# Optimization experiments

Measured on AMD Instinct MI355X. Metric: run time of the kernel, lower is better.

## Reference

```python
import jax, jax.numpy as jnp
import numpy as np

EMBED = 1024
HEADS = 16
HEAD_DIM = EMBED // HEADS


def setup_inputs() -> dict:
    key = jax.random.key(0)
    ks = jax.random.split(key, 9)
    N, L = 2, 2048
    inp = {
        "values": jax.random.normal(ks[0], (N, L, EMBED), dtype=jnp.float32),
        "keys": jax.random.normal(ks[1], (N, L, EMBED), dtype=jnp.float32),
        "query": jax.random.normal(ks[2], (N, L, EMBED), dtype=jnp.float32),
        "mask": jax.random.randint(ks[3], (N, 1, L, L), 0, 2, dtype=jnp.int32),
        # per-head projection weights (torch Linear: y = x @ W.T), bias=False
        "Wv": jax.random.normal(ks[4], (HEAD_DIM, HEAD_DIM), dtype=jnp.float32) / np.sqrt(HEAD_DIM),
        "Wk": jax.random.normal(ks[5], (HEAD_DIM, HEAD_DIM), dtype=jnp.float32) / np.sqrt(HEAD_DIM),
        "Wq": jax.random.normal(ks[6], (HEAD_DIM, HEAD_DIM), dtype=jnp.float32) / np.sqrt(HEAD_DIM),
        "Wo": jax.random.normal(ks[7], (EMBED, EMBED), dtype=jnp.float32) / np.sqrt(EMBED),
        "bo": jax.random.normal(ks[8], (EMBED,), dtype=jnp.float32) * 0.02,
    }
    return inp


def reference(values, keys, query, mask, Wv, Wk, Wq, Wo, bo):
    N, Lq = query.shape[0], query.shape[1]
    Lk = keys.shape[1]
    # reshape to (N, L, H, D)
    v = values.reshape(N, Lk, HEADS, HEAD_DIM)
    k = keys.reshape(N, Lk, HEADS, HEAD_DIM)
    q = query.reshape(N, Lq, HEADS, HEAD_DIM)
    # per-head_dim linear projections (shared across heads): x @ W.T
    v = jnp.einsum('nlhd,ed->nlhe', v, Wv)
    k = jnp.einsum('nlhd,ed->nlhe', k, Wk)
    q = jnp.einsum('nqhd,ed->nqhe', q, Wq)
    # scores [N, H, Lq, Lk]
    energy = jnp.einsum('nqhd,nkhd->nhqk', q, k) / np.sqrt(HEAD_DIM).astype(np.float32)
    energy = jnp.where(mask == 0, jnp.float32(-1e20), energy)
    attn = jax.nn.softmax(energy, axis=-1)
    out = jnp.einsum('nhql,nlhd->nqhd', attn, v).reshape(N, Lq, EMBED)
    return out @ Wo.T + bo
```

## Files before the change

### kernel.cpp

```cpp
#include <hip/hip_runtime.h>
#include <hip/hip_bf16.h>

#define SEQ 2048
#define NH 16
#define DH 64
#define EMB 1024

typedef __bf16 bf16;
typedef __attribute__((ext_vector_type(8))) __bf16 bf16x8;
typedef __attribute__((ext_vector_type(4))) __bf16 bf16x4;
typedef __attribute__((ext_vector_type(4))) float f32x4;
typedef __attribute__((ext_vector_type(4))) unsigned int u32x4;
typedef unsigned long long u64;

#define OFF_MQK  0
#define OFF_WO2  8192
#define OFF_K2   (8192 + 2097152)
#define OFF_VT   (OFF_K2 + 8388608)
#define OFF_A2   (OFF_VT + 8388608)
#define OFF_MB   (OFF_A2 + 8388608)

#define LOG2E 1.44269504088896340736f

__device__ __forceinline__ f32x4 mfma16(bf16x8 a, bf16x8 b, f32x4 c) {
  return __builtin_amdgcn_mfma_f32_16x16x32_bf16(a, b, c, 0, 0, 0);
}

#define GL16(g, l)                                                            \
  __builtin_amdgcn_global_load_lds(                                           \
      (const __attribute__((address_space(1))) void*)(g),                     \
      (__attribute__((address_space(3))) void*)(l), 16, 0, 0)

__device__ __forceinline__ unsigned pack_bf16(float p0, float p1) {
  unsigned short b0 = __builtin_bit_cast(unsigned short, (bf16)p0);
  unsigned short b1 = __builtin_bit_cast(unsigned short, (bf16)p1);
  return (unsigned)b0 | ((unsigned)b1 << 16);
}

__global__ __launch_bounds__(256) void prep0(const float* __restrict__ Wq,
                                             const float* __restrict__ Wk,
                                             bf16* __restrict__ mqk) {
  __shared__ float wq[64 * 64];
  __shared__ float wk[64 * 64];
  int tid = threadIdx.x;
  for (int i = tid; i < 4096; i += 256) { wq[i] = Wq[i]; wk[i] = Wk[i]; }
  __syncthreads();
  for (int idx = tid; idx < 4096; idx += 256) {
    int d1 = idx >> 6, d2 = idx & 63;
    float s = 0.f;
#pragma unroll
    for (int e = 0; e < 64; ++e) s += wq[e * 64 + d1] * wk[e * 64 + d2];
    mqk[idx] = (bf16)(s * 0.125f * LOG2E);
  }
}

__global__ __launch_bounds__(256) void prep_fused(
    const float* __restrict__ Wo, const float* __restrict__ Wv,
    const float* __restrict__ keys, const bf16* __restrict__ mqk,
    const float* __restrict__ values, const int* __restrict__ mask,
    bf16* __restrict__ wo2f, bf16* __restrict__ k2f, bf16* __restrict__ vtf,
    u64* __restrict__ mbt) {
  __shared__ __align__(16) float smem[5184];
  int blk = blockIdx.x;
  int tid = threadIdx.x;

  if (blk < 1024) {
    int e = blk;
    float* wv = smem;
    float* worow = smem + 4096;
    for (int i = tid; i < 4096; i += 256) wv[i] = Wv[i];
    for (int i = tid; i < 1024; i += 256) worow[i] = Wo[(size_t)e * 1024 + i];
    __syncthreads();
    int c0 = tid * 4;
    bf16x4 w;
#pragma unroll
    for (int j = 0; j < 4; ++j) {
      int col = c0 + j;
      int hb = col & ~63, dp = col & 63;
      float s = 0.f;
#pragma unroll
      for (int d = 0; d < 64; ++d) s += worow[hb + d] * wv[d * 64 + dp];
      w[j] = (bf16)s;
    }
    int et = e >> 6, t = (e >> 4) & 3, cc = e & 15;
    int kc = c0 >> 5, gg = (c0 >> 3) & 3, half = (c0 >> 2) & 1;
    char* dst = (char*)wo2f + ((size_t)(et * 32 + kc)) * 4096 + t * 1024 +
                (gg * 16 + cc) * 16 + 8 * half;
    *(bf16x4*)dst = w;
  } else if (blk < 2048) {
    int b = blk - 1024;
    int lt = b & 31, h = (b >> 5) & 15, n = b >> 9;
    int wave = tid >> 6, lane = tid & 63;
    int g = lane >> 4, c = lane & 15;
    bf16x8 am[4][2];
#pragma unroll
    for (int t = 0; t < 4; ++t)
#pragma unroll
      for (int s = 0; s < 2; ++s)
        am[t][s] = *(const bf16x8*)(mqk + (16 * t + c) * 64 + 32 * s + 8 * g);
    int l = lt * 64 + wave * 16 + c;
    const float* krow = keys + ((size_t)(n * SEQ + l)) * EMB + h * DH;
    bf16x8 bfr[2];
#pragma unroll
    for (int s = 0; s < 2; ++s) {
      f32x4 x0 = *(const f32x4*)(krow + 32 * s + 8 * g);
      f32x4 x1 = *(const f32x4*)(krow + 32 * s + 8 * g + 4);
      bf16x8 t;
#pragma unroll
      for (int i = 0; i < 4; ++i) { t[i] = (bf16)x0[i]; t[4 + i] = (bf16)x1[i]; }
      bfr[s] = t;
    }
    char* tb = (char*)k2f + (size_t)((n * NH + h) * 32 + lt) * 8192 + wave * 2048;
#pragma unroll
    for (int t = 0; t < 4; ++t) {
      f32x4 a = {0.f, 0.f, 0.f, 0.f};
      a = mfma16(am[t][0], bfr[0], a);
      a = mfma16(am[t][1], bfr[1], a);
      bf16x4 w;
#pragma unroll
      for (int r = 0; r < 4; ++r) w[r] = (bf16)a[r];
      char* dst = tb + (t >> 1) * 1024 +
                  ((2 * (t & 1) + (g >> 1)) * 16 + c) * 16 + 8 * (g & 1);
      *(bf16x4*)dst = w;
    }
  } else if (blk < 3072) {
    int b = blk - 2048;
    int lt = b & 31, h = (b >> 5) & 15, n = b >> 9;
    float (*lds)[65] = (float(*)[65])smem;
    {
      int r = tid >> 2, cg = (tid & 3) * 16;
      const float* vrow =
          values + ((size_t)(n * SEQ + lt * 64 + r)) * EMB + h * DH + cg;
#pragma unroll
      for (int j = 0; j < 16; j += 4) {
        f32x4 x = *(const f32x4*)(vrow + j);
        lds[r][cg + j + 0] = x[0];
        lds[r][cg + j + 1] = x[1];
        lds[r][cg + j + 2] = x[2];
        lds[r][cg + j + 3] = x[3];
      }
    }
    __syncthreads();
    {
      int d = tid >> 2, q16 = tid & 3, lb = q16 * 16;
      bf16x8 w0, w1;
#pragma unroll
      for (int j = 0; j < 8; ++j) w0[j] = (bf16)lds[lb + j][d];
#pragma unroll
      for (int j = 0; j < 8; ++j) w1[j] = (bf16)lds[lb + 8 + j][d];
      int dt = d >> 4, cc = d & 15;
      int s = q16 >> 1, gg = 2 * (q16 & 1);
      char* base = (char*)vtf + (size_t)((n * NH + h) * 32 + lt) * 8192 +
                   (2 * dt + s) * 1024;
      *(bf16x8*)(base + (gg * 16 + cc) * 16) = w0;
      *(bf16x8*)(base + ((gg + 1) * 16 + cc) * 16) = w1;
    }
  } else {
    int base = (blk - 3072) * 4 + (tid >> 6);
    int lane = tid & 63;
#pragma unroll
    for (int i = 0; i < 16; ++i) {
      int w = base + i * 8192;
      int v = mask[(size_t)w * 64 + lane];
      u64 bbits = __ballot(v != 0);
      int kw = w & 31, q = (w >> 5) & 2047, nn = w >> 16;
      if (lane == 0) mbt[((size_t)nn * 32 + kw) * 2048 + q] = bbits;
    }
  }
}

__global__ __launch_bounds__(64, 2) void attn(const float* __restrict__ qraw,
                                              const bf16* __restrict__ k2f,
                                              const bf16* __restrict__ vtf,
                                              const u64* __restrict__ mbt,
                                              bf16* __restrict__ a2) {
  int swz = ((blockIdx.x & 7) << 8) | (blockIdx.x >> 3);
  int qt = swz & 63, h = (swz >> 6) & 15, n = swz >> 10;
  int lane = threadIdx.x, g = lane >> 4, c = lane & 15;

  __shared__ u64 lutm[16];
  if (lane < 16) {
    unsigned a = (lane & 1 ? 0xFFFFu : 0u) | (lane & 2 ? 0xFFFF0000u : 0u);
    unsigned b = (lane & 4 ? 0xFFFFu : 0u) | (lane & 8 ? 0xFFFF0000u : 0u);
    lutm[lane] = (u64)a | ((u64)b << 32);
  }
  __syncthreads();

  bf16x8 qf[2][2];
#pragma unroll
  for (int qi = 0; qi < 2; ++qi) {
    int q = qt * 32 + qi * 16 + c;
    const float* qrow = qraw + ((size_t)(n * SEQ + q)) * EMB + h * DH;
#pragma unroll
    for (int s = 0; s < 2; ++s) {
      f32x4 x0 = *(const f32x4*)(qrow + 32 * s + 8 * g);
      f32x4 x1 = *(const f32x4*)(qrow + 32 * s + 8 * g + 4);
      bf16x8 t;
#pragma unroll
      for (int i = 0; i < 4; ++i) { t[i] = (bf16)x0[i]; t[4 + i] = (bf16)x1[i]; }
      qf[qi][s] = t;
    }
  }
  const char* kp = (const char*)k2f + (size_t)(n * NH + h) * 32 * 8192 + lane * 16;
  const char* vp = (const char*)vtf + (size_t)(n * NH + h) * 32 * 8192 + lane * 16;
  const u64* mq = mbt + (size_t)n * 32 * 2048 + qt * 32 + c;

  bf16x8 K[8], Vv[8];
#pragma unroll
  for (int j = 0; j < 8; ++j) K[j] = *(const bf16x8*)(kp + j * 1024);

  f32x4 oacc[2][4];
#pragma unroll
  for (int qi = 0; qi < 2; ++qi)
#pragma unroll
    for (int dt = 0; dt < 4; ++dt) oacc[qi][dt] = (f32x4){0.f, 0.f, 0.f, 0.f};
  float mrun[2] = {-1e30f, -1e30f}, lrun[2] = {0.f, 0.f};
  bf16x8 ones;
#pragma unroll
  for (int i = 0; i < 8; ++i) ones[i] = (bf16)1.0f;
  int sh0 = 4 * g, sh1 = sh0 + 16;
  int srcA = ((g & 1) << 5) | c;
  int srcB = srcA + 16;
  bool hi2 = (g >> 1) != 0;

  for (int kt = 0; kt < 32; ++kt) {
#pragma unroll
    for (int j = 0; j < 8; ++j)
      Vv[j] = *(const bf16x8*)(vp + (size_t)kt * 8192 + j * 1024);
    u64 mw0 = mq[kt * 2048];
    u64 mw1 = mq[kt * 2048 + 16];

    f32x4 sacc[2][4];
#pragma unroll
    for (int t = 0; t < 4; ++t) {
      bf16x8 k0 = K[2 * t], k1 = K[2 * t + 1];
#pragma unroll
      for (int qi = 0; qi < 2; ++qi) {
        f32x4 a = {0.f, 0.f, 0.f, 0.f};
        a = mfma16(k0, qf[qi][0], a);
        a = mfma16(k1, qf[qi][1], a);
        sacc[qi][t] = a;
      }
    }
#pragma unroll
    for (int j = 0; j < 8; ++j)
      K[j] = *(const bf16x8*)(kp + (size_t)(kt + 1) * 8192 + j * 1024);

    float tmax[2];
#pragma unroll
    for (int qi = 0; qi < 2; ++qi) {
      float x0 = sacc[qi][0][0], x1 = sacc[qi][0][1], x2 = sacc[qi][0][2],
            x3 = sacc[qi][0][3], x4 = sacc[qi][1][0], x5 = sacc[qi][1][1],
            x6 = sacc[qi][1][2], x7 = sacc[qi][1][3], x8 = sacc[qi][2][0],
            x9 = sacc[qi][2][1], xa = sacc[qi][2][2], xb = sacc[qi][2][3],
            xc = sacc[qi][3][0], xd = sacc[qi][3][1], xe = sacc[qi][3][2],
            xf = sacc[qi][3][3];
      float t0 = fmaxf(fmaxf(x0, x1), x2);
      float t1 = fmaxf(fmaxf(x3, x4), x5);
      float t2 = fmaxf(fmaxf(x6, x7), x8);
      float t3 = fmaxf(fmaxf(x9, xa), xb);
      float t4 = fmaxf(fmaxf(xc, xd), xe);
      float m = fmaxf(fmaxf(fmaxf(t0, t1), t2), fmaxf(fmaxf(t3, t4), xf));
      m = fmaxf(m, __shfl_xor(m, 16));
      m = fmaxf(m, __shfl_xor(m, 32));
      tmax[qi] = m;
    }
    bool needs = (tmax[0] > mrun[0] + 8.f) || (tmax[1] > mrun[1] + 8.f);
    if (__any(needs)) {
#pragma unroll
      for (int qi = 0; qi < 2; ++qi) {
        float mnew = fmaxf(mrun[qi], tmax[qi]);
        float scl = __builtin_amdgcn_exp2f(mrun[qi] - mnew);
        lrun[qi] *= scl;
#pragma unroll
        for (int dt = 0; dt < 4; ++dt) {
          oacc[qi][dt][0] *= scl; oacc[qi][dt][1] *= scl;
          oacc[qi][dt][2] *= scl; oacc[qi][dt][3] *= scl;
        }
        mrun[qi] = mnew;
      }
    }
    unsigned wpk[2][4][2];
    u64 mwa[2] = {mw0, mw1};
#pragma unroll
    for (int qi = 0; qi < 2; ++qi) {
      unsigned mlo = (unsigned)mwa[qi], mhi = (unsigned)(mwa[qi] >> 32);
      u64 L[4];
      L[0] = lutm[(mlo >> sh0) & 15];
      L[1] = lutm[(mlo >> sh1) & 15];
      L[2] = lutm[(mhi >> sh0) & 15];
      L[3] = lutm[(mhi >> sh1) & 15];
      float mr = mrun[qi];
#pragma unroll
      for (int t = 0; t < 4; ++t) {
        float p0 = __builtin_amdgcn_exp2f(sacc[qi][t][0] - mr);
        float p1 = __builtin_amdgcn_exp2f(sacc[qi][t][1] - mr);
        float p2 = __builtin_amdgcn_exp2f(sacc[qi][t][2] - mr);
        float p3 = __builtin_amdgcn_exp2f(sacc[qi][t][3] - mr);
        wpk[qi][t][0] = pack_bf16(p0, p1) & (unsigned)L[t];
        wpk[qi][t][1] = pack_bf16(p2, p3) & (unsigned)(L[t] >> 32);
      }
    }
    bf16x8 pf[2][2];
#pragma unroll
    for (int qi = 0; qi < 2; ++qi)
#pragma unroll
      for (int s = 0; s < 2; ++s) {
        unsigned ta0 = (unsigned)__shfl((int)wpk[qi][2 * s][0], srcA);
        unsigned ta1 = (unsigned)__shfl((int)wpk[qi][2 * s][1], srcA);
        unsigned tb0 = (unsigned)__shfl((int)wpk[qi][2 * s + 1][0], srcA);
        unsigned tb1 = (unsigned)__shfl((int)wpk[qi][2 * s + 1][1], srcA);
        unsigned ua0 = (unsigned)__shfl((int)wpk[qi][2 * s][0], srcB);
        unsigned ua1 = (unsigned)__shfl((int)wpk[qi][2 * s][1], srcB);
        unsigned ub0 = (unsigned)__shfl((int)wpk[qi][2 * s + 1][0], srcB);
        unsigned ub1 = (unsigned)__shfl((int)wpk[qi][2 * s + 1][1], srcB);
        u32x4 f;
        f[0] = hi2 ? tb0 : ta0;
        f[1] = hi2 ? tb1 : ta1;
        f[2] = hi2 ? ub0 : ua0;
        f[3] = hi2 ? ub1 : ua1;
        pf[qi][s] = __builtin_bit_cast(bf16x8, f);
      }
    f32x4 pacc[2];
#pragma unroll
    for (int qi = 0; qi < 2; ++qi) {
      f32x4 a = {0.f, 0.f, 0.f, 0.f};
      a = mfma16(ones, pf[qi][0], a);
      a = mfma16(ones, pf[qi][1], a);
      pacc[qi] = a;
    }
#pragma unroll
    for (int dt = 0; dt < 4; ++dt)
#pragma unroll
      for (int s = 0; s < 2; ++s) {
        bf16x8 vf = Vv[2 * dt + s];
#pragma unroll
        for (int qi = 0; qi < 2; ++qi)
          oacc[qi][dt] = mfma16(vf, pf[qi][s], oacc[qi][dt]);
      }
#pragma unroll
    for (int qi = 0; qi < 2; ++qi) lrun[qi] += pacc[qi][0];
  }
#pragma unroll
  for (int qi = 0; qi < 2; ++qi) {
    float inv = 1.0f / lrun[qi];
    int q = qt * 32 + qi * 16 + c;
    bf16* orow = a2 + ((size_t)(n * SEQ + q)) * EMB + h * DH;
#pragma unroll
    for (int dt = 0; dt < 4; ++dt) {
      bf16x4 w2;
#pragma unroll
      for (int r = 0; r < 4; ++r) w2[r] = (bf16)(oacc[qi][dt][r] * inv);
      *(bf16x4*)(orow + 16 * dt + 4 * g) = w2;
    }
  }
}

__global__ __launch_bounds__(256) void out_gemm(const bf16* __restrict__ a2,
                                                const bf16* __restrict__ wo2f,
                                                const float* __restrict__ bo,
                                                float* __restrict__ out) {
  int blk = blockIdx.x;
  int et = blk & 15, mt = blk >> 4;
  int tid = threadIdx.x, wave = tid >> 6, lane = tid & 63;
  int g = lane >> 4, c = lane & 15;
  int m = mt * 64 + wave * 16 + c;
  const bf16* arow = a2 + (size_t)m * EMB + 8 * g;

  __shared__ bf16 wbuf[2][4096];
  const char* wtile = (const char*)wo2f + (size_t)et * 32 * 4096;
  int lofs = lane * 16, wofs = wave * 1024;

#define STAGEW(J, BUF)                                                        \
  {                                                                           \
    const char* src_ = wtile + (size_t)(J) * 8192 + wofs + lofs;              \
    char* dst_ = (char*)&wbuf[BUF][0] + wofs;                                 \
    GL16(src_, dst_);                                                         \
    GL16(src_ + 4096, dst_ + 4096);                                           \
  }

  STAGEW(0, 0);
  bf16x8 bn0 = *(const bf16x8*)(arow);
  bf16x8 bn1 = *(const bf16x8*)(arow + 32);
  __syncthreads();

  f32x4 acc[4];
#pragma unroll
  for (int t = 0; t < 4; ++t) acc[t] = (f32x4){0.f, 0.f, 0.f, 0.f};

  for (int j = 0; j < 16; ++j) {
    int cur = j & 1;
    bf16x8 b0 = bn0, b1 = bn1;
    if (j < 15) {
      STAGEW(j + 1, cur ^ 1);
      bn0 = *(const bf16x8*)(arow + (j + 1) * 64);
      bn1 = *(const bf16x8*)(arow + (j + 1) * 64 + 32);
    }
    const bf16* wb = &wbuf[cur][0];
#pragma unroll
    for (int t = 0; t < 4; ++t)
      acc[t] = mfma16(*(const bf16x8*)(wb + t * 512 + lane * 8), b0, acc[t]);
#pragma unroll
    for (int t = 0; t < 4; ++t)
      acc[t] =
          mfma16(*(const bf16x8*)(wb + 2048 + t * 512 + lane * 8), b1, acc[t]);
    __syncthreads();
  }
#pragma unroll
  for (int t = 0; t < 4; ++t) {
    int e = et * 64 + 16 * t + 4 * g;
    f32x4 b = *(const f32x4*)(bo + e);
    f32x4 w;
#pragma unroll
    for (int r = 0; r < 4; ++r) w[r] = acc[t][r] + b[r];
    *(f32x4*)(out + (size_t)m * EMB + e) = w;
  }
}

extern "C" void kernel_launch(void* const* d_in, const int* in_sizes, int n_in,
                              void* d_out, int out_size, void* d_ws, size_t ws_size,
                              hipStream_t stream) {
  const float* values = (const float*)d_in[0];
  const float* keys   = (const float*)d_in[1];
  const float* query  = (const float*)d_in[2];
  const int*   mask   = (const int*)d_in[3];
  const float* Wv     = (const float*)d_in[4];
  const float* Wk     = (const float*)d_in[5];
  const float* Wq     = (const float*)d_in[6];
  const float* Wo     = (const float*)d_in[7];
  const float* bo     = (const float*)d_in[8];

  char* ws = (char*)d_ws;
  bf16* mqk  = (bf16*)(ws + OFF_MQK);
  bf16* wo2f = (bf16*)(ws + OFF_WO2);
  bf16* k2f  = (bf16*)(ws + OFF_K2);
  bf16* vtf  = (bf16*)(ws + OFF_VT);
  bf16* a2   = (bf16*)(ws + OFF_A2);
  u64*  mbt  = (u64*)(ws + OFF_MB);

  prep0<<<1, 256, 0, stream>>>(Wq, Wk, mqk);
  prep_fused<<<5120, 256, 0, stream>>>(Wo, Wv, keys, mqk, values, mask,
                                       wo2f, k2f, vtf, mbt);
  attn<<<2048, 64, 0, stream>>>(query, k2f, vtf, mbt, a2);
  out_gemm<<<1024, 256, 0, stream>>>(a2, wo2f, bo, (float*)d_out);
}
```

Before: 126.1 us.

## Compute Wo·Wv fold with MFMA, parallelize prep0, double out_gemm K-step

The Wo×Wv weight fold used to run as scalar FP32 dot products, one block per output row. It now uses 256 blocks that each run bf16 MFMA tiles on a transposed Wv held in LDS. prep0 now spreads the Wq·Wk product over 16 blocks instead of one. out_gemm stages 128-wide K chunks (8 iterations instead of 16), which halves the number of barriers and stage issues in exchange for twice the LDS. The fold now rounds its inputs to bf16, which adds a small precision change.

```diff
diff --git a/kernel.cpp b/kernel.cpp
--- a/kernel.cpp
+++ b/kernel.cpp
@@ -42,16 +42,14 @@
                                              bf16* __restrict__ mqk) {
   __shared__ float wq[64 * 64];
   __shared__ float wk[64 * 64];
-  int tid = threadIdx.x;
+  int tid = threadIdx.x, b = blockIdx.x;
   for (int i = tid; i < 4096; i += 256) { wq[i] = Wq[i]; wk[i] = Wk[i]; }
   __syncthreads();
-  for (int idx = tid; idx < 4096; idx += 256) {
-    int d1 = idx >> 6, d2 = idx & 63;
-    float s = 0.f;
-#pragma unroll
-    for (int e = 0; e < 64; ++e) s += wq[e * 64 + d1] * wk[e * 64 + d2];
-    mqk[idx] = (bf16)(s * 0.125f * LOG2E);
-  }
+  int d1 = b * 4 + (tid >> 6), d2 = tid & 63;
+  float s = 0.f;
+#pragma unroll
+  for (int e = 0; e < 64; ++e) s += wq[e * 64 + d1] * wk[e * 64 + d2];
+  mqk[d1 * 64 + d2] = (bf16)(s * 0.125f * LOG2E);
 }
 
 __global__ __launch_bounds__(256) void prep_fused(
@@ -64,31 +62,54 @@
   int blk = blockIdx.x;
   int tid = threadIdx.x;
 
-  if (blk < 1024) {
-    int e = blk;
-    float* wv = smem;
-    float* worow = smem + 4096;
-    for (int i = tid; i < 4096; i += 256) wv[i] = Wv[i];
-    for (int i = tid; i < 1024; i += 256) worow[i] = Wo[(size_t)e * 1024 + i];
+  if (blk < 256) {
+    int h = blk >> 4, eg = blk & 15;
+    int wave = tid >> 6, lane = tid & 63;
+    int g = lane >> 4, c = lane & 15;
+    float (*wvT)[65] = (float(*)[65])smem;
+    for (int i = tid; i < 4096; i += 256) {
+      int d = i >> 6, dp = i & 63;
+      wvT[dp][d] = Wv[i];
+    }
     __syncthreads();
-    int c0 = tid * 4;
-    bf16x4 w;
-#pragma unroll
-    for (int j = 0; j < 4; ++j) {
-      int col = c0 + j;
-      int hb = col & ~63, dp = col & 63;
-      float s = 0.f;
-#pragma unroll
-      for (int d = 0; d < 64; ++d) s += worow[hb + d] * wv[d * 64 + dp];
-      w[j] = (bf16)s;
-    }
-    int et = e >> 6, t = (e >> 4) & 3, cc = e & 15;
-    int kc = c0 >> 5, gg = (c0 >> 3) & 3, half = (c0 >> 2) & 1;
-    char* dst = (char*)wo2f + ((size_t)(et * 32 + kc)) * 4096 + t * 1024 +
-                (gg * 16 + cc) * 16 + 8 * half;
-    *(bf16x4*)dst = w;
-  } else if (blk < 2048) {
-    int b = blk - 1024;
+    bf16x8 am[4][2];
+#pragma unroll
+    for (int t = 0; t < 4; ++t)
+#pragma unroll
+      for (int s = 0; s < 2; ++s) {
+        bf16x8 v;
+#pragma unroll
+        for (int i = 0; i < 8; ++i)
+          v[i] = (bf16)wvT[16 * t + c][32 * s + 8 * g + i];
+        am[t][s] = v;
+      }
+    int e = eg * 64 + wave * 16 + c;
+    const float* worow = Wo + (size_t)e * 1024 + h * DH;
+    bf16x8 bfr[2];
+#pragma unroll
+    for (int s = 0; s < 2; ++s) {
+      f32x4 x0 = *(const f32x4*)(worow + 32 * s + 8 * g);
+      f32x4 x1 = *(const f32x4*)(worow + 32 * s + 8 * g + 4);
+      bf16x8 t;
+#pragma unroll
+      for (int i = 0; i < 4; ++i) { t[i] = (bf16)x0[i]; t[4 + i] = (bf16)x1[i]; }
+      bfr[s] = t;
+    }
+    char* tb = (char*)wo2f + (size_t)(eg * 32 + h * 2) * 4096 + wave * 1024;
+#pragma unroll
+    for (int t = 0; t < 4; ++t) {
+      f32x4 a = {0.f, 0.f, 0.f, 0.f};
+      a = mfma16(am[t][0], bfr[0], a);
+      a = mfma16(am[t][1], bfr[1], a);
+      bf16x4 w;
+#pragma unroll
+      for (int r = 0; r < 4; ++r) w[r] = (bf16)a[r];
+      char* dst = tb + (t >> 1) * 4096 +
+                  ((2 * (t & 1) + (g >> 1)) * 16 + c) * 16 + 8 * (g & 1);
+      *(bf16x4*)dst = w;
+    }
+  } else if (blk < 1280) {
+    int b = blk - 256;
     int lt = b & 31, h = (b >> 5) & 15, n = b >> 9;
     int wave = tid >> 6, lane = tid & 63;
     int g = lane >> 4, c = lane & 15;
@@ -123,8 +144,8 @@
                   ((2 * (t & 1) + (g >> 1)) * 16 + c) * 16 + 8 * (g & 1);
       *(bf16x4*)dst = w;
     }
-  } else if (blk < 3072) {
-    int b = blk - 2048;
+  } else if (blk < 2304) {
+    int b = blk - 1280;
     int lt = b & 31, h = (b >> 5) & 15, n = b >> 9;
     float (*lds)[65] = (float(*)[65])smem;
     {
@@ -156,7 +177,7 @@
       *(bf16x8*)(base + ((gg + 1) * 16 + cc) * 16) = w1;
     }
   } else {
-    int base = (blk - 3072) * 4 + (tid >> 6);
+    int base = (blk - 2304) * 4 + (tid >> 6);
     int lane = tid & 63;
 #pragma unroll
     for (int i = 0; i < 16; ++i) {
@@ -367,34 +388,38 @@
   int m = mt * 64 + wave * 16 + c;
   const bf16* arow = a2 + (size_t)m * EMB + 8 * g;
 
-  __shared__ bf16 wbuf[2][4096];
+  __shared__ bf16 wbuf[2][8192];
   const char* wtile = (const char*)wo2f + (size_t)et * 32 * 4096;
   int lofs = lane * 16, wofs = wave * 1024;
 
 #define STAGEW(J, BUF)                                                        \
   {                                                                           \
-    const char* src_ = wtile + (size_t)(J) * 8192 + wofs + lofs;              \
+    const char* src_ = wtile + (size_t)(J) * 16384 + wofs + lofs;             \
     char* dst_ = (char*)&wbuf[BUF][0] + wofs;                                 \
     GL16(src_, dst_);                                                         \
     GL16(src_ + 4096, dst_ + 4096);                                           \
+    GL16(src_ + 8192, dst_ + 8192);                                           \
+    GL16(src_ + 12288, dst_ + 12288);                                         \
   }
 
   STAGEW(0, 0);
-  bf16x8 bn0 = *(const bf16x8*)(arow);
-  bf16x8 bn1 = *(const bf16x8*)(arow + 32);
+  bf16x8 bn[4];
+#pragma unroll
+  for (int q = 0; q < 4; ++q) bn[q] = *(const bf16x8*)(arow + q * 32);
   __syncthreads();
 
   f32x4 acc[4];
 #pragma unroll
   for (int t = 0; t < 4; ++t) acc[t] = (f32x4){0.f, 0.f, 0.f, 0.f};
 
-  for (int j = 0; j < 16; ++j) {
+  for (int j = 0; j < 8; ++j) {
     int cur = j & 1;
-    bf16x8 b0 = bn0, b1 = bn1;
-    if (j < 15) {
+    bf16x8 b0 = bn[0], b1 = bn[1], b2 = bn[2], b3 = bn[3];
+    if (j < 7) {
       STAGEW(j + 1, cur ^ 1);
-      bn0 = *(const bf16x8*)(arow + (j + 1) * 64);
-      bn1 = *(const bf16x8*)(arow + (j + 1) * 64 + 32);
+#pragma unroll
+      for (int q = 0; q < 4; ++q)
+        bn[q] = *(const bf16x8*)(arow + (j + 1) * 128 + q * 32);
     }
     const bf16* wb = &wbuf[cur][0];
 #pragma unroll
@@ -404,6 +429,14 @@
     for (int t = 0; t < 4; ++t)
       acc[t] =
           mfma16(*(const bf16x8*)(wb + 2048 + t * 512 + lane * 8), b1, acc[t]);
+#pragma unroll
+    for (int t = 0; t < 4; ++t)
+      acc[t] =
+          mfma16(*(const bf16x8*)(wb + 4096 + t * 512 + lane * 8), b2, acc[t]);
+#pragma unroll
+    for (int t = 0; t < 4; ++t)
+      acc[t] =
+          mfma16(*(const bf16x8*)(wb + 6144 + t * 512 + lane * 8), b3, acc[t]);
     __syncthreads();
   }
 #pragma unroll
@@ -438,8 +471,8 @@
   bf16* a2   = (bf16*)(ws + OFF_A2);
   u64*  mbt  = (u64*)(ws + OFF_MB);
 
-  prep0<<<1, 256, 0, stream>>>(Wq, Wk, mqk);
-  prep_fused<<<5120, 256, 0, stream>>>(Wo, Wv, keys, mqk, values, mask,
+  prep0<<<16, 256, 0, stream>>>(Wq, Wk, mqk);
+  prep_fused<<<4352, 256, 0, stream>>>(Wo, Wv, keys, mqk, values, mask,
                                        wo2f, k2f, vtf, mbt);
   attn<<<2048, 64, 0, stream>>>(query, k2f, vtf, mbt, a2);
   out_gemm<<<1024, 256, 0, stream>>>(a2, wo2f, bo, (float*)d_out);
```

Result: faster. 114.9 us (-8.9%).
